# Kernel tuning notes

Measured on AMD Instinct MI355X. Metric: run time of the kernel, lower is better.

## Reference

```python
import jax, jax.numpy as jnp
import numpy as np

N_NODES = 50000
N_EDGES = 800000
D_IN = 128
D_OUT = 128
K = 3


def setup_inputs() -> dict:
    key = jax.random.key(0)
    k1, k2, k3, k4 = jax.random.split(key, 4)
    x = jax.random.normal(k1, (N_NODES, D_IN), dtype=jnp.float32)
    W = jax.random.normal(k2, (K, D_IN, D_OUT), dtype=jnp.float32) * 0.05
    edge_index = jax.random.randint(k3, (K, 2, N_EDGES), 0, N_NODES, dtype=jnp.int32)
    edge_weight = jax.random.uniform(k4, (K, N_EDGES), dtype=jnp.float32)
    return {"x": x, "W": W, "edge_index": edge_index, "edge_weight": edge_weight}


def reference(x, W, edge_index, edge_weight):
    # ChebConv: out = sum_k A_k @ (x @ W_k), A_k given as weighted edge lists.
    n = x.shape[0]
    out = jnp.zeros((n, W.shape[-1]), dtype=x.dtype)
    for k in range(W.shape[0]):
        h = x @ W[k]                                   # [N, D_OUT] dense GEMM
        src = edge_index[k, 0]
        dst = edge_index[k, 1]
        msg = h[src] * edge_weight[k][:, None]         # [E, D_OUT] gather + scale
        out = out + jax.ops.segment_sum(msg, dst, num_segments=n)
    return out
```

## Files before the change

kernel.cpp:

```cpp
#include <hip/hip_runtime.h>
#include <hip/hip_bf16.h>

#define N_NODES 50000
#define N_EDGES 800000
#define D 128
#define KCHEB 3
#define NBKT 98
#define TOTB (KCHEB * NBKT)
#define SLAB 16384
#define EPB 4096
#define NBLK_E ((N_EDGES + EPB - 1) / EPB)

typedef __attribute__((ext_vector_type(8))) short short8v;
typedef __attribute__((ext_vector_type(4))) float f32x4;

__device__ inline unsigned f2bf(float f) {
    unsigned x = __float_as_uint(f);
    unsigned r = ((x >> 16) & 1u) + 0x7FFFu;
    return (x + r) >> 16;
}

__global__ __launch_bounds__(256) void wprep(const float* __restrict__ W,
                                             unsigned short* __restrict__ Wtg) {
    const int k = blockIdx.x;
    const float* Wk = W + (size_t)k * D * D;
    unsigned short* o = Wtg + (size_t)k * D * D;
    for (int i = threadIdx.x; i < 4096; i += 256) {
        int r  = i >> 5;
        int c4 = (i & 31) * 4;
        float4 wv = *(const float4*)&Wk[r * 128 + c4];
        #pragma unroll
        for (int j = 0; j < 4; ++j) {
            int row = c4 + j;
            int byte_in_row = (r * 2) ^ ((row & 7) << 4);
            o[row * 128 + (byte_in_row >> 1)] = (unsigned short)f2bf((&wv.x)[j]);
        }
    }
}

__global__ __launch_bounds__(256) void gemm_mfma(const float* __restrict__ x,
                                                 const unsigned short* __restrict__ Wtg,
                                                 unsigned* __restrict__ h3, int n) {
    __shared__ unsigned short Wt[128 * 128];
    const int t = threadIdx.x;
    unsigned* h2 = h3 + (size_t)blockIdx.y * N_NODES * 64;

    {
        const uint4* src = (const uint4*)(Wtg + (size_t)blockIdx.y * D * D);
        uint4* dst = (uint4*)Wt;
        #pragma unroll
        for (int i = 0; i < 8; ++i) dst[t + 256 * i] = src[t + 256 * i];
    }
    __syncthreads();

    const int lane = t & 63, w = t >> 6;
    const int m0 = blockIdx.x * 64 + w * 16;
    const int arow = m0 + (lane & 15);
    const float* xr = x + (size_t)(arow < n ? arow : 0) * D + ((lane >> 4) << 3);

    short8v afr[4];
    #pragma unroll
    for (int kt = 0; kt < 4; ++kt) {
        float4 p0 = *(const float4*)(xr + kt * 32);
        float4 p1 = *(const float4*)(xr + kt * 32 + 4);
        union { short8v s; unsigned u[4]; } a;
        a.u[0] = f2bf(p0.x) | (f2bf(p0.y) << 16);
        a.u[1] = f2bf(p0.z) | (f2bf(p0.w) << 16);
        a.u[2] = f2bf(p1.x) | (f2bf(p1.y) << 16);
        a.u[3] = f2bf(p1.z) | (f2bf(p1.w) << 16);
        afr[kt] = a.s;
    }

    f32x4 acc[8] = {};
    const int kb = (lane >> 4) << 4;
    #pragma unroll
    for (int nn = 0; nn < 8; ++nn) {
        const int row = nn * 16 + (lane & 15);
        const int sw = (row & 7) << 4;
        const unsigned short* wr = &Wt[row * 128];
        #pragma unroll
        for (int kt = 0; kt < 4; ++kt) {
            int byte_in_row = ((kt << 6) + kb) ^ sw;
            short8v b = *(const short8v*)&wr[byte_in_row >> 1];
            acc[nn] = __builtin_amdgcn_mfma_f32_16x16x32_bf16(afr[kt], b, acc[nn], 0, 0, 0);
        }
    }

    unsigned short* hs = (unsigned short*)h2;
    const int orow_base = m0 + ((lane >> 4) << 2);
    const int col_base = lane & 15;
    #pragma unroll
    for (int nn = 0; nn < 8; ++nn) {
        int col = nn * 16 + col_base;
        #pragma unroll
        for (int r = 0; r < 4; ++r) {
            int orow = orow_base + r;
            if (orow < n) hs[(size_t)orow * D + col] = (unsigned short)f2bf(acc[nn][r]);
        }
    }
}

__global__ __launch_bounds__(1024) void bucket_bin(const int* __restrict__ ei,
                                                   const float* __restrict__ ew,
                                                   int* __restrict__ cursor,
                                                   uint2* __restrict__ binned) {
    __shared__ int lh[NBKT], gb[NBKT], lc[NBKT];
    const int k = blockIdx.y, t = threadIdx.x;
    for (int i = t; i < NBKT; i += 1024) { lh[i] = 0; lc[i] = 0; }
    __syncthreads();
    const int* srcs = ei + (size_t)k * 2 * N_EDGES;
    const int* dsts = srcs + N_EDGES;
    const float* w = ew + (size_t)k * N_EDGES;
    const int e = blockIdx.x * EPB + t * 4;

    if (e < N_EDGES) {
        int4 d4 = *(const int4*)&dsts[e];
        atomicAdd(&lh[d4.x >> 9], 1);
        atomicAdd(&lh[d4.y >> 9], 1);
        atomicAdd(&lh[d4.z >> 9], 1);
        atomicAdd(&lh[d4.w >> 9], 1);
    }
    __syncthreads();
    for (int i = t; i < NBKT; i += 1024)
        gb[i] = lh[i] ? atomicAdd(&cursor[k * NBKT + i], lh[i]) : 0;
    __syncthreads();
    if (e < N_EDGES) {
        int4 d4 = *(const int4*)&dsts[e];
        int4 s4 = *(const int4*)&srcs[e];
        float4 w4 = *(const float4*)&w[e];
        #pragma unroll
        for (int j = 0; j < 4; ++j) {
            int d = (&d4.x)[j];
            int b = d >> 9;
            int pos = (k * NBKT + b) * SLAB + gb[b] + atomicAdd(&lc[b], 1);
            binned[pos] = make_uint2(__float_as_uint((&w4.x)[j]),
                                     (unsigned)(&s4.x)[j] | ((unsigned)(d & 511) << 16));
        }
    }
}

__global__ __launch_bounds__(1024) void build_csr(const uint2* __restrict__ binned,
                                                  const int* __restrict__ cursor,
                                                  int* __restrict__ off,
                                                  int* __restrict__ num,
                                                  unsigned* __restrict__ csr4) {
    __shared__ int nh[512], ex[512], wsum[4];
    const int kb = blockIdx.x;
    const int k = kb / NBKT, b = kb % NBKT;
    const int t = threadIdx.x;
    const int beg = kb * SLAB;
    const int end = beg + cursor[kb];

    for (int i = t; i < 512; i += 1024) nh[i] = 0;
    __syncthreads();
    for (int i = beg + t; i < end; i += 1024)
        atomicAdd(&nh[(binned[i].y >> 16) & 511], 1);
    __syncthreads();

    if (t < 256) {
        int a0 = nh[2 * t], a1 = nh[2 * t + 1];
        int s = a0 + a1;
        int lane = t & 63, wid = t >> 6;
        int v = s;
        #pragma unroll
        for (int d = 1; d < 64; d <<= 1) {
            int u = __shfl_up(v, d, 64);
            if (lane >= d) v += u;
        }
        if (lane == 63) wsum[wid] = v;
        __syncthreads();
        int wb = 0;
        for (int i = 0; i < wid; ++i) wb += wsum[i];
        int ep = wb + v - s;
        ex[2 * t] = ep;
        ex[2 * t + 1] = ep + a0;

        const int node0 = b * 512;
        int n0 = node0 + 2 * t, n1 = node0 + 2 * t + 1;
        if (n0 < N_NODES) { off[k * N_NODES + n0] = beg + ep;      num[k * N_NODES + n0] = a0; }
        if (n1 < N_NODES) { off[k * N_NODES + n1] = beg + ep + a0; num[k * N_NODES + n1] = a1; }
    } else {
        __syncthreads();
    }
    for (int i = t; i < 512; i += 1024) nh[i] = 0;
    __syncthreads();
    for (int i = beg + t; i < end; i += 1024) {
        uint2 e = binned[i];
        int dl = (e.y >> 16) & 511;
        int pos = beg + ex[dl] + atomicAdd(&nh[dl], 1);
        csr4[pos] = (e.y & 0xFFFFu) | (f2bf(__uint_as_float(e.x)) << 16);
    }
}

__global__ __launch_bounds__(256) void gather_all(const unsigned* __restrict__ h3,
                                                  const unsigned* __restrict__ csr4,
                                                  const int* __restrict__ off,
                                                  const int* __restrict__ num,
                                                  float* __restrict__ out) {
    const int half = threadIdx.x >> 5;
    const int l = threadIdx.x & 31;
    const int node = blockIdx.x * 8 + half;
    if (node >= N_NODES) return;

    float a0 = 0.f, a1 = 0.f, a2 = 0.f, a3 = 0.f;
    #pragma unroll
    for (int k = 0; k < KCHEB; ++k) {
        const unsigned* h2 = h3 + (size_t)k * N_NODES * 64;
        const int kd = k * N_NODES + node;
        int i = off[kd];
        const int end = i + num[kd];
        for (; i + 8 <= end; i += 8) {
            unsigned e[8];
            uint2 u[8];
            #pragma unroll
            for (int j = 0; j < 8; ++j) e[j] = csr4[i + j];
            #pragma unroll
            for (int j = 0; j < 8; ++j)
                u[j] = *(const uint2*)&h2[(size_t)(e[j] & 0xFFFFu) * 64 + l * 2];
            #pragma unroll
            for (int j = 0; j < 8; ++j) {
                float w = __uint_as_float(e[j] & 0xFFFF0000u);
                a0 += w * __uint_as_float(u[j].x << 16);
                a1 += w * __uint_as_float(u[j].x & 0xFFFF0000u);
                a2 += w * __uint_as_float(u[j].y << 16);
                a3 += w * __uint_as_float(u[j].y & 0xFFFF0000u);
            }
        }
        for (; i < end; ++i) {
            unsigned e = csr4[i];
            float w = __uint_as_float(e & 0xFFFF0000u);
            uint2 u = *(const uint2*)&h2[(size_t)(e & 0xFFFFu) * 64 + l * 2];
            a0 += w * __uint_as_float(u.x << 16);
            a1 += w * __uint_as_float(u.x & 0xFFFF0000u);
            a2 += w * __uint_as_float(u.y << 16);
            a3 += w * __uint_as_float(u.y & 0xFFFF0000u);
        }
    }
    *(float4*)&out[(size_t)node * D + l * 4] = make_float4(a0, a1, a2, a3);
}

extern "C" void kernel_launch(void* const* d_in, const int* in_sizes, int n_in,
                              void* d_out, int out_size, void* d_ws, size_t ws_size,
                              hipStream_t stream) {
    const float* x  = (const float*)d_in[0];
    const float* W  = (const float*)d_in[1];
    const int*   ei = (const int*)d_in[2];
    const float* ew = (const float*)d_in[3];
    float* out = (float*)d_out;

    char* ws = (char*)d_ws;
    unsigned*       csr4   = (unsigned*)      (ws);
    uint2*          binned = (uint2*)         (ws + 19267584);
    unsigned*       h3     = (unsigned*)      (ws + 57802752);
    int*            off    = (int*)           (ws + 96202752);
    int*            num    = (int*)           (ws + 96802752);
    int*            cursor = (int*)           (ws + 97402752);
    unsigned short* Wtg    = (unsigned short*)(ws + 97403936);

    hipMemsetAsync(cursor, 0, TOTB * sizeof(int), stream);

    wprep<<<KCHEB, 256, 0, stream>>>(W, Wtg);

    const dim3 egrid(NBLK_E, KCHEB);
    bucket_bin<<<egrid, 1024, 0, stream>>>(ei, ew, cursor, binned);

    const dim3 ggrid((N_NODES + 63) / 64, KCHEB);
    gemm_mfma<<<ggrid, 256, 0, stream>>>(x, Wtg, h3, N_NODES);

    build_csr<<<TOTB, 1024, 0, stream>>>(binned, cursor, off, num, csr4);

    const int gat_grid = (N_NODES + 7) / 8;
    gather_all<<<gat_grid, 256, 0, stream>>>(h3, csr4, off, num, out);
}
```

Baseline: 252.5 us.

## Vectorize GEMM output stores, fold memset, reuse loads, predicate gather tail

Swaps the MFMA operand order so each lane holds four consecutive output columns of one node, which allows 8-byte packed bf16 stores instead of scattered 2-byte stores. The cursor memset is folded into the wprep kernel, removing one API call. bucket_bin now loads edge data once and keeps it in registers across the barrier instead of reloading it. The gather's scalar tail loop is replaced by a predicated 8-wide batch, which adds some wasted loads for low-degree nodes.

```diff
diff --git a/kernel.cpp b/kernel.cpp
--- a/kernel.cpp
+++ b/kernel.cpp
@@ -21,8 +21,11 @@
 }
 
 __global__ __launch_bounds__(256) void wprep(const float* __restrict__ W,
-                                             unsigned short* __restrict__ Wtg) {
+                                             unsigned short* __restrict__ Wtg,
+                                             int* __restrict__ cursor) {
     const int k = blockIdx.x;
+    if (k == 0)
+        for (int i = threadIdx.x; i < TOTB; i += 256) cursor[i] = 0;
     const float* Wk = W + (size_t)k * D * D;
     unsigned short* o = Wtg + (size_t)k * D * D;
     for (int i = threadIdx.x; i < 4096; i += 256) {
@@ -82,20 +85,19 @@
         for (int kt = 0; kt < 4; ++kt) {
             int byte_in_row = ((kt << 6) + kb) ^ sw;
             short8v b = *(const short8v*)&wr[byte_in_row >> 1];
-            acc[nn] = __builtin_amdgcn_mfma_f32_16x16x32_bf16(afr[kt], b, acc[nn], 0, 0, 0);
-        }
-    }
-
-    unsigned short* hs = (unsigned short*)h2;
-    const int orow_base = m0 + ((lane >> 4) << 2);
-    const int col_base = lane & 15;
-    #pragma unroll
-    for (int nn = 0; nn < 8; ++nn) {
-        int col = nn * 16 + col_base;
-        #pragma unroll
-        for (int r = 0; r < 4; ++r) {
-            int orow = orow_base + r;
-            if (orow < n) hs[(size_t)orow * D + col] = (unsigned short)f2bf(acc[nn][r]);
+            acc[nn] = __builtin_amdgcn_mfma_f32_16x16x32_bf16(b, afr[kt], acc[nn], 0, 0, 0);
+        }
+    }
+
+    const int node = m0 + (lane & 15);
+    if (node < n) {
+        unsigned short* hs = (unsigned short*)h2;
+        const int g4 = (lane >> 4) << 2;
+        #pragma unroll
+        for (int nn = 0; nn < 8; ++nn) {
+            unsigned lo = f2bf(acc[nn][0]) | (f2bf(acc[nn][1]) << 16);
+            unsigned hi = f2bf(acc[nn][2]) | (f2bf(acc[nn][3]) << 16);
+            *(uint2*)&hs[(size_t)node * D + nn * 16 + g4] = make_uint2(lo, hi);
         }
     }
 }
@@ -112,9 +114,14 @@
     const int* dsts = srcs + N_EDGES;
     const float* w = ew + (size_t)k * N_EDGES;
     const int e = blockIdx.x * EPB + t * 4;
-
-    if (e < N_EDGES) {
-        int4 d4 = *(const int4*)&dsts[e];
+    const bool ok = e < N_EDGES;
+
+    int4 d4 = make_int4(0, 0, 0, 0), s4 = make_int4(0, 0, 0, 0);
+    float4 w4 = make_float4(0.f, 0.f, 0.f, 0.f);
+    if (ok) {
+        d4 = *(const int4*)&dsts[e];
+        s4 = *(const int4*)&srcs[e];
+        w4 = *(const float4*)&w[e];
         atomicAdd(&lh[d4.x >> 9], 1);
         atomicAdd(&lh[d4.y >> 9], 1);
         atomicAdd(&lh[d4.z >> 9], 1);
@@ -124,10 +131,7 @@
     for (int i = t; i < NBKT; i += 1024)
         gb[i] = lh[i] ? atomicAdd(&cursor[k * NBKT + i], lh[i]) : 0;
     __syncthreads();
-    if (e < N_EDGES) {
-        int4 d4 = *(const int4*)&dsts[e];
-        int4 s4 = *(const int4*)&srcs[e];
-        float4 w4 = *(const float4*)&w[e];
+    if (ok) {
         #pragma unroll
         for (int j = 0; j < 4; ++j) {
             int d = (&d4.x)[j];
@@ -207,33 +211,28 @@
     for (int k = 0; k < KCHEB; ++k) {
         const unsigned* h2 = h3 + (size_t)k * N_NODES * 64;
         const int kd = k * N_NODES + node;
-        int i = off[kd];
-        const int end = i + num[kd];
-        for (; i + 8 <= end; i += 8) {
+        const int i0 = off[kd];
+        const int cnt = num[kd];
+        for (int b0 = 0; b0 < cnt; b0 += 8) {
             unsigned e[8];
             uint2 u[8];
+            float wv[8];
             #pragma unroll
-            for (int j = 0; j < 8; ++j) e[j] = csr4[i + j];
+            for (int j = 0; j < 8; ++j) {
+                bool okj = (b0 + j) < cnt;
+                e[j] = csr4[okj ? i0 + b0 + j : i0];
+                wv[j] = okj ? __uint_as_float(e[j] & 0xFFFF0000u) : 0.f;
+            }
             #pragma unroll
             for (int j = 0; j < 8; ++j)
                 u[j] = *(const uint2*)&h2[(size_t)(e[j] & 0xFFFFu) * 64 + l * 2];
             #pragma unroll
             for (int j = 0; j < 8; ++j) {
-                float w = __uint_as_float(e[j] & 0xFFFF0000u);
-                a0 += w * __uint_as_float(u[j].x << 16);
-                a1 += w * __uint_as_float(u[j].x & 0xFFFF0000u);
-                a2 += w * __uint_as_float(u[j].y << 16);
-                a3 += w * __uint_as_float(u[j].y & 0xFFFF0000u);
+                a0 += wv[j] * __uint_as_float(u[j].x << 16);
+                a1 += wv[j] * __uint_as_float(u[j].x & 0xFFFF0000u);
+                a2 += wv[j] * __uint_as_float(u[j].y << 16);
+                a3 += wv[j] * __uint_as_float(u[j].y & 0xFFFF0000u);
             }
-        }
-        for (; i < end; ++i) {
-            unsigned e = csr4[i];
-            float w = __uint_as_float(e & 0xFFFF0000u);
-            uint2 u = *(const uint2*)&h2[(size_t)(e & 0xFFFFu) * 64 + l * 2];
-            a0 += w * __uint_as_float(u.x << 16);
-            a1 += w * __uint_as_float(u.x & 0xFFFF0000u);
-            a2 += w * __uint_as_float(u.y << 16);
-            a3 += w * __uint_as_float(u.y & 0xFFFF0000u);
         }
     }
     *(float4*)&out[(size_t)node * D + l * 4] = make_float4(a0, a1, a2, a3);
@@ -257,9 +256,7 @@
     int*            cursor = (int*)           (ws + 97402752);
     unsigned short* Wtg    = (unsigned short*)(ws + 97403936);
 
-    hipMemsetAsync(cursor, 0, TOTB * sizeof(int), stream);
-
-    wprep<<<KCHEB, 256, 0, stream>>>(W, Wtg);
+    wprep<<<KCHEB, 256, 0, stream>>>(W, Wtg, cursor);
 
     const dim3 egrid(NBLK_E, KCHEB);
     bucket_bin<<<egrid, 1024, 0, stream>>>(ei, ew, cursor, binned);
```

Measured after the change: 251.0 us. Within noise of the previous version (-0.6%).
